# Optimization experiments

Measured on AMD Instinct MI355X. Metric: run time of the kernel, lower is better.

Reference implementation:

```python
import jax, jax.numpy as jnp
import numpy as np

BN_EPS = 1e-5


def setup_inputs() -> dict:
    key = jax.random.key(0)
    ks = jax.random.split(key, 6)
    N, E, D_IN, D_OUT = 100000, 625000, 128, 128
    x = jax.random.normal(ks[0], (N, D_IN), dtype=jnp.float32)
    edge_index = jax.random.randint(ks[1], (2, E), 0, N, dtype=jnp.int64)
    # Glorot-style init for GCNConv weight, uniform for linear (values only matter for correctness testing)
    W = jax.random.normal(ks[2], (D_IN, D_OUT), dtype=jnp.float32) * (1.0 / np.sqrt(D_IN))
    b = jnp.zeros((D_OUT,), dtype=jnp.float32)
    res_W = jax.random.normal(ks[3], (D_IN, D_OUT), dtype=jnp.float32) * (1.0 / np.sqrt(D_IN))
    res_b = jnp.zeros((D_OUT,), dtype=jnp.float32)
    bn_gamma = jnp.ones((D_OUT,), dtype=jnp.float32)
    bn_beta = jnp.zeros((D_OUT,), dtype=jnp.float32)
    return {"x": x, "edge_index": edge_index, "W": W, "b": b,
            "res_W": res_W, "res_b": res_b, "bn_gamma": bn_gamma, "bn_beta": bn_beta}


def _gcn_forward(x, edge_index, W, b, res_W, res_b, bn_gamma, bn_beta):
    N = x.shape[0]
    # ---- GCNConv: add self-loops, symmetric degree normalization (PyG defaults) ----
    loops = jnp.arange(N, dtype=edge_index.dtype)
    src = jnp.concatenate([edge_index[0], loops])  # row (source)
    dst = jnp.concatenate([edge_index[1], loops])  # col (target)
    ones = jnp.ones(src.shape[0], dtype=x.dtype)
    deg = jax.ops.segment_sum(ones, dst, num_segments=N)  # in-degree incl. self-loop
    deg_inv_sqrt = jnp.where(deg > 0, jax.lax.rsqrt(deg), 0.0)
    norm = deg_inv_sqrt[src] * deg_inv_sqrt[dst]  # [E+N]
    # transform first (dense GEMM), then gather/scale/scatter-add
    h = x @ W  # [N, D_OUT]
    msg = h[src] * norm[:, None]  # gather + scale
    agg = jax.ops.segment_sum(msg, dst, num_segments=N) + b  # scatter-add + bias
    # ---- residual: relu(linear(x)) ----
    res = jax.nn.relu(x @ res_W + res_b)
    y = agg + res
    # ---- dropout(p=0.0) is identity; BatchNorm1d (training mode, batch stats) ----
    mean = jnp.mean(y, axis=0)
    var = jnp.mean(jnp.square(y - mean), axis=0)  # biased variance, as in torch BN normalization
    y = (y - mean) * jax.lax.rsqrt(var + BN_EPS) * bn_gamma + bn_beta
    return y


def reference(x, edge_index, W, b, res_W, res_b, bn_gamma, bn_beta):
    return _gcn_forward(x, edge_index, W, b, res_W, res_b, bn_gamma, bn_beta)
```

## Files before the change

kernel.cpp:

```cpp
#include <hip/hip_runtime.h>
#include <math.h>

#define D 128

typedef __attribute__((ext_vector_type(8))) short bf16x8;
typedef __attribute__((ext_vector_type(4))) float f32x4;
union U4 { uint4 u; bf16x8 f; };

__device__ __forceinline__ float blo(unsigned p){ return __uint_as_float(p << 16); }
__device__ __forceinline__ float bhi(unsigned p){ return __uint_as_float(p & 0xffff0000u); }
__device__ __forceinline__ unsigned bpack(float a, float b){
  unsigned x = __float_as_uint(a), y = __float_as_uint(b);
  x += 0x7fffu + ((x >> 16) & 1u);
  y += 0x7fffu + ((y >> 16) & 1u);
  return (x >> 16) | (y & 0xffff0000u);
}


__global__ void k_deg(const int* __restrict__ ei, int* __restrict__ cnt, int E){
  int e = blockIdx.x*256 + threadIdx.x;
  if (e < E) atomicAdd(cnt + ei[E + e], 1);
}

__global__ void k_scan1(const int* __restrict__ cnt, int* __restrict__ off,
                        int* __restrict__ bsum, int N){
  __shared__ int sm[256];
  int i = blockIdx.x*256 + threadIdx.x;
  int v = (i < N) ? cnt[i] : 0;
  int acc = v;
  sm[threadIdx.x] = acc;
  __syncthreads();
  for (int s = 1; s < 256; s <<= 1){
    int t = (threadIdx.x >= s) ? sm[threadIdx.x - s] : 0;
    __syncthreads();
    acc += t;
    sm[threadIdx.x] = acc;
    __syncthreads();
  }
  if (i < N) off[i] = acc - v;
  if (threadIdx.x == 255) bsum[blockIdx.x] = acc;
}

__global__ void k_scan2(int* __restrict__ bsum, int nb){
  __shared__ int sm[512];
  int v = (threadIdx.x < nb) ? bsum[threadIdx.x] : 0;
  int acc = v;
  sm[threadIdx.x] = acc;
  __syncthreads();
  for (int s = 1; s < 512; s <<= 1){
    int t = (threadIdx.x >= s) ? sm[threadIdx.x - s] : 0;
    __syncthreads();
    acc += t;
    sm[threadIdx.x] = acc;
    __syncthreads();
  }
  if (threadIdx.x < nb) bsum[threadIdx.x] = acc - v;
}

__global__ void k_scan3(int* __restrict__ off, const int* __restrict__ bsum,
                        int* __restrict__ cursor, int N){
  int i = blockIdx.x*256 + threadIdx.x;
  if (i < N){
    int o = off[i] + bsum[blockIdx.x];
    off[i] = o;
    cursor[i] = o;
  }
}

__global__ void k_prep(const float* __restrict__ x, const int* __restrict__ cnt,
                       unsigned* __restrict__ out_u, int N){
  int idx = blockIdx.x*256 + threadIdx.x;
  if (idx >= N*32) return;
  int row = idx >> 5, q = idx & 31;
  float dis = rsqrtf((float)(cnt[row] + 1));
  float4 xv = reinterpret_cast<const float4*>(x)[idx];
  uint2 r; r.x = bpack(xv.x*dis, xv.y*dis); r.y = bpack(xv.z*dis, xv.w*dis);
  reinterpret_cast<uint2*>(out_u)[(size_t)row*64 + 32 + q] = r;
}

__global__ void k_wprep(const float* __restrict__ W, const float* __restrict__ RW,
                        unsigned* __restrict__ dst){
  int idx = blockIdx.x*256 + threadIdx.x;
  int m = idx >> 13;
  int w = idx & 8191;
  int c = w >> 6, kd = w & 63;
  const float* src = m ? RW : W;
  float a = src[(2*kd)*128 + c];
  float b = src[(2*kd+1)*128 + c];
  dst[(m<<13) + c*64 + (kd ^ ((c & 7) << 2))] = bpack(a, b);
}

__global__ void k_fill(const int* __restrict__ ei, int* __restrict__ cursor,
                       int* __restrict__ elist, int E){
  int e = blockIdx.x*256 + threadIdx.x;
  if (e < E){
    int d = ei[E + e];
    int pos = atomicAdd(cursor + d, 1);
    elist[pos] = ei[e];
  }
}

__global__ __launch_bounds__(256) void k_agg(unsigned* __restrict__ out_u,
    const int* __restrict__ elist, const int* __restrict__ off,
    const int* __restrict__ cnt, int N){
  const int lane = threadIdx.x & 63;
  int wid = blockIdx.x*4 + (threadIdx.x >> 6);
  const int nw = gridDim.x*4;
  for (int i = wid; i < N; i += nw){
    int node = __builtin_amdgcn_readfirstlane(i);
    int o = off[node];
    int c = cnt[node];
    unsigned ps = out_u[(size_t)node*128 + 64 + lane];
    float a0 = 0.f, a1 = 0.f;
    for (int j0 = 0; j0 < c; j0 += 64){
      int m = c - j0; if (m > 64) m = 64;
      int li = lane < m ? lane : m-1;
      int sid = elist[o + j0 + li];
      for (int jj = 0; jj < m; jj += 4){
        int s0 = __shfl(sid, jj);
        int s1 = __shfl(sid, jj+1 < m ? jj+1 : m-1);
        int s2 = __shfl(sid, jj+2 < m ? jj+2 : m-1);
        int s3 = __shfl(sid, jj+3 < m ? jj+3 : m-1);
        unsigned p0 = out_u[(size_t)s0*128 + 64 + lane];
        unsigned p1 = out_u[(size_t)s1*128 + 64 + lane];
        unsigned p2 = out_u[(size_t)s2*128 + 64 + lane];
        unsigned p3 = out_u[(size_t)s3*128 + 64 + lane];
        if (jj+1 >= m) p1 = 0;
        if (jj+2 >= m) p2 = 0;
        if (jj+3 >= m) p3 = 0;
        a0 += blo(p0) + blo(p1) + blo(p2) + blo(p3);
        a1 += bhi(p0) + bhi(p1) + bhi(p2) + bhi(p3);
      }
    }
    a0 += blo(ps); a1 += bhi(ps);
    float dis = rsqrtf((float)(c + 1));
    out_u[(size_t)node*128 + lane] = bpack(a0*dis, a1*dis);
  }
}

__global__ __launch_bounds__(512) void k_gemm(
    const unsigned* __restrict__ wsW,
    const float* __restrict__ bias, const float* __restrict__ rbias,
    const int* __restrict__ cnt,
    float* __restrict__ out, float* __restrict__ colsum, int N)
{
  __shared__ unsigned lds[16384];
  unsigned* out_u = reinterpret_cast<unsigned*>(out);
  for (int i = threadIdx.x; i < 16384; i += 512) lds[i] = wsW[i];
  __syncthreads();

  const int lane = threadIdx.x & 63;
  const int wave = threadIdx.x >> 6;
  const int lo = lane & 15, hi = lane >> 4;
  const int rowbase = blockIdx.x * 128 + wave * 16;

  int arow = rowbase + lo; if (arow >= N) arow = N - 1;
  U4 aggF[4], xbF[4];
  #pragma unroll
  for (int kk = 0; kk < 4; ++kk){
    aggF[kk].u = *(const uint4*)&out_u[(size_t)arow*128 + kk*16 + hi*4];
    xbF[kk].u  = *(const uint4*)&out_u[(size_t)arow*128 + 64 + kk*16 + hi*4];
  }

  f32x4 accA[8], accR[8];
  #pragma unroll
  for (int ct = 0; ct < 8; ++ct){
    accA[ct] = (f32x4){0.f,0.f,0.f,0.f};
    accR[ct] = (f32x4){0.f,0.f,0.f,0.f};
  }
  #pragma unroll
  for (int ct = 0; ct < 8; ++ct){
    const int c = ct*16 + lo;
    #pragma unroll
    for (int kk = 0; kk < 4; ++kk){
      int kd = (kk*16 + hi*4) ^ ((c & 7) << 2);
      U4 wf, rf;
      wf.u = *(const uint4*)&lds[c*64 + kd];
      rf.u = *(const uint4*)&lds[8192 + c*64 + kd];
      accA[ct] = __builtin_amdgcn_mfma_f32_16x16x32_bf16(aggF[kk].f, wf.f, accA[ct], 0,0,0);
      accR[ct] = __builtin_amdgcn_mfma_f32_16x16x32_bf16(xbF[kk].f, rf.f, accR[ct], 0,0,0);
    }
  }

  float s_[4];
  #pragma unroll
  for (int j = 0; j < 4; ++j){
    int r = rowbase + hi*4 + j;
    int rc = r < N ? r : N - 1;
    s_[j] = sqrtf((float)(cnt[rc] + 1));
  }
  const int rb4 = rowbase + hi*4;
  float cs[8], cq[8];
  #pragma unroll
  for (int ct = 0; ct < 8; ++ct){
    cs[ct] = 0.f; cq[ct] = 0.f;
    float bc  = bias[ct*16 + lo];
    float rbc = rbias[ct*16 + lo];
    #pragma unroll
    for (int j = 0; j < 4; ++j){
      float y = accA[ct][j] + bc + fmaxf(accR[ct][j]*s_[j] + rbc, 0.f);
      if (rb4 + j < N){ cs[ct] += y; cq[ct] += y*y; }
      accA[ct][j] = y;
    }
  }

  __syncthreads();
  float* yl = reinterpret_cast<float*>(lds);
  #pragma unroll
  for (int ct = 0; ct < 8; ++ct){
    #pragma unroll
    for (int j = 0; j < 4; ++j)
      yl[(wave*16 + hi*4 + j)*128 + ct*16 + lo] = accA[ct][j];
  }
  __syncthreads();

  const int rbB = blockIdx.x * 128;
  #pragma unroll
  for (int chunk = 0; chunk < 16; ++chunk){
    int g = chunk*512 + threadIdx.x;
    int lr = g >> 6, d = g & 63;
    int row = rbB + lr;
    if (row < N){
      float a = yl[lr*128 + 2*d], b = yl[lr*128 + 2*d + 1];
      out_u[(size_t)row*128 + d] = bpack(a, b);
    }
  }

  #pragma unroll
  for (int ct = 0; ct < 8; ++ct){
    cs[ct] += __shfl_xor(cs[ct], 16); cs[ct] += __shfl_xor(cs[ct], 32);
    cq[ct] += __shfl_xor(cq[ct], 16); cq[ct] += __shfl_xor(cq[ct], 32);
  }
  __syncthreads();
  float* red = reinterpret_cast<float*>(lds);
  if (lane < 16){
    #pragma unroll
    for (int ct = 0; ct < 8; ++ct){
      int col = ct*16 + lane;
      red[wave*256 + 2*col]     = cs[ct];
      red[wave*256 + 2*col + 1] = cq[ct];
    }
  }
  __syncthreads();
  if (threadIdx.x < 256){
    float t = 0.f;
    #pragma unroll
    for (int w = 0; w < 8; ++w) t += red[w*256 + threadIdx.x];
    atomicAdd(colsum + threadIdx.x, t);
  }
}

__global__ __launch_bounds__(256) void k_norm(float* out, const float* __restrict__ colsum,
                       const float* __restrict__ gamma, const float* __restrict__ beta,
                       float fN, int N){
  __shared__ float sc[256];
  if (threadIdx.x < 128){
    int c = threadIdx.x;
    float mean = colsum[2*c] / fN;
    float var  = fmaxf(colsum[2*c + 1] / fN - mean*mean, 0.f);
    float s = gamma[c] * rsqrtf(var + 1e-5f);
    sc[c] = s;
    sc[128 + c] = beta[c] - mean * s;
  }
  __syncthreads();
  const int lane = threadIdx.x & 63;
  const int wv   = threadIdx.x >> 6;
  unsigned* out_u = reinterpret_cast<unsigned*>(out);
  const int rowsPerIter = gridDim.x * 16;
  for (int r0 = (blockIdx.x*4 + wv)*4; r0 < N; r0 += rowsPerIter){
    int rr = r0 + (lane >> 4);
    int d  = (lane & 15) * 4;
    if (rr < N){
      uint4 p = *reinterpret_cast<uint4*>(&out_u[(size_t)rr*128 + d]);
      int c0 = d*2;
      float4 o1, o2;
      o1.x = blo(p.x)*sc[c0+0] + sc[128+c0+0];
      o1.y = bhi(p.x)*sc[c0+1] + sc[128+c0+1];
      o1.z = blo(p.y)*sc[c0+2] + sc[128+c0+2];
      o1.w = bhi(p.y)*sc[c0+3] + sc[128+c0+3];
      o2.x = blo(p.z)*sc[c0+4] + sc[128+c0+4];
      o2.y = bhi(p.z)*sc[c0+5] + sc[128+c0+5];
      o2.z = blo(p.w)*sc[c0+6] + sc[128+c0+6];
      o2.w = bhi(p.w)*sc[c0+7] + sc[128+c0+7];
      *reinterpret_cast<float4*>(&out[(size_t)rr*128 + c0])     = o1;
      *reinterpret_cast<float4*>(&out[(size_t)rr*128 + c0 + 4]) = o2;
    }
  }
}

extern "C" void kernel_launch(void* const* d_in, const int* in_sizes, int n_in,
                              void* d_out, int out_size, void* d_ws, size_t ws_size,
                              hipStream_t stream){
  const float* x     = (const float*)d_in[0];
  const int*   ei    = (const int*)d_in[1];
  const float* W     = (const float*)d_in[2];
  const float* b     = (const float*)d_in[3];
  const float* RW    = (const float*)d_in[4];
  const float* rb    = (const float*)d_in[5];
  const float* gamma = (const float*)d_in[6];
  const float* beta  = (const float*)d_in[7];
  float* out = (float*)d_out;
  unsigned* out_u = (unsigned*)d_out;
  const int N = in_sizes[0] / D;
  const int E = in_sizes[1] / 2;

  char* ws = (char*)d_ws;
  size_t o = 0;
  auto alloc = [&](size_t bytes)->void*{
    void* p = ws + o;
    o += (bytes + 255) & ~size_t(255);
    return p;
  };
  int*      cnt    = (int*)alloc((size_t)N*4);
  int*      off    = (int*)alloc((size_t)N*4);
  int*      cursor = (int*)alloc((size_t)N*4);
  int*      bsum   = (int*)alloc(512*4);
  float*    colsum = (float*)alloc(256*4);
  unsigned* wsW    = (unsigned*)alloc(16384*4);
  int*      elist  = (int*)alloc((size_t)E*4);

  hipMemsetAsync(cnt, 0, (size_t)N*4, stream);
  hipMemsetAsync(colsum, 0, 256*4, stream);

  int egrid = (E + 255)/256;
  int nb = (N + 255)/256;
  k_deg  <<<egrid, 256, 0, stream>>>(ei, cnt, E);
  k_scan1<<<nb,    256, 0, stream>>>(cnt, off, bsum, N);
  k_scan2<<<1,     512, 0, stream>>>(bsum, nb);
  k_scan3<<<nb,    256, 0, stream>>>(off, bsum, cursor, N);
  k_prep <<<(N*32 + 255)/256, 256, 0, stream>>>(x, cnt, out_u, N);
  k_wprep<<<64,    256, 0, stream>>>(W, RW, wsW);
  k_fill <<<egrid, 256, 0, stream>>>(ei, cursor, elist, E);
  k_agg  <<<4096,  256, 0, stream>>>(out_u, elist, off, cnt, N);
  k_gemm <<<(N + 127)/128, 512, 0, stream>>>(wsW, b, rb, cnt, out, colsum, N);
  k_norm <<<2048,  256, 0, stream>>>(out, colsum, gamma, beta, (float)N, N);
}
```

Before: 271.6 us.

## Fuse prep kernels, shard CSR fill by destination, and widen aggregation loads

```diff
diff --git a/kernel.cpp b/kernel.cpp
--- a/kernel.cpp
+++ b/kernel.cpp
@@ -22,8 +22,21 @@
   if (e < E) atomicAdd(cnt + ei[E + e], 1);
 }
 
-__global__ void k_scan1(const int* __restrict__ cnt, int* __restrict__ off,
-                        int* __restrict__ bsum, int N){
+__global__ void k_scan1w(const int* __restrict__ cnt, int* __restrict__ off,
+                         int* __restrict__ bsum, int N, int nb,
+                         const float* __restrict__ W, const float* __restrict__ RW,
+                         unsigned* __restrict__ wdst){
+  if (blockIdx.x >= nb){
+    int idx = (blockIdx.x - nb)*256 + threadIdx.x;
+    int m = idx >> 13;
+    int w = idx & 8191;
+    int c = w >> 6, kd = w & 63;
+    const float* src = m ? RW : W;
+    float a = src[(2*kd)*128 + c];
+    float b = src[(2*kd+1)*128 + c];
+    wdst[(m<<13) + c*64 + (kd ^ ((c & 7) << 2))] = bpack(a, b);
+    return;
+  }
   __shared__ int sm[256];
   int i = blockIdx.x*256 + threadIdx.x;
   int v = (i < N) ? cnt[i] : 0;
@@ -57,46 +70,36 @@
   if (threadIdx.x < nb) bsum[threadIdx.x] = acc - v;
 }
 
-__global__ void k_scan3(int* __restrict__ off, const int* __restrict__ bsum,
-                        int* __restrict__ cursor, int N){
-  int i = blockIdx.x*256 + threadIdx.x;
-  if (i < N){
-    int o = off[i] + bsum[blockIdx.x];
-    off[i] = o;
-    cursor[i] = o;
-  }
-}
-
-__global__ void k_prep(const float* __restrict__ x, const int* __restrict__ cnt,
-                       unsigned* __restrict__ out_u, int N){
+__global__ void k_prep3(const float* __restrict__ x, const int* __restrict__ cnt,
+                        const int* __restrict__ bsum, int* __restrict__ off,
+                        int* __restrict__ cursor, unsigned* __restrict__ out_u, int N){
   int idx = blockIdx.x*256 + threadIdx.x;
   if (idx >= N*32) return;
   int row = idx >> 5, q = idx & 31;
+  if (q == 0){
+    int o = off[row] + bsum[row >> 8];
+    off[row] = o;
+    cursor[row] = o;
+  }
   float dis = rsqrtf((float)(cnt[row] + 1));
   float4 xv = reinterpret_cast<const float4*>(x)[idx];
   uint2 r; r.x = bpack(xv.x*dis, xv.y*dis); r.y = bpack(xv.z*dis, xv.w*dis);
   reinterpret_cast<uint2*>(out_u)[(size_t)row*64 + 32 + q] = r;
 }
 
-__global__ void k_wprep(const float* __restrict__ W, const float* __restrict__ RW,
-                        unsigned* __restrict__ dst){
-  int idx = blockIdx.x*256 + threadIdx.x;
-  int m = idx >> 13;
-  int w = idx & 8191;
-  int c = w >> 6, kd = w & 63;
-  const float* src = m ? RW : W;
-  float a = src[(2*kd)*128 + c];
-  float b = src[(2*kd+1)*128 + c];
-  dst[(m<<13) + c*64 + (kd ^ ((c & 7) << 2))] = bpack(a, b);
-}
-
-__global__ void k_fill(const int* __restrict__ ei, int* __restrict__ cursor,
-                       int* __restrict__ elist, int E){
-  int e = blockIdx.x*256 + threadIdx.x;
-  if (e < E){
+__global__ __launch_bounds__(256) void k_fill(const int* __restrict__ ei,
+    int* __restrict__ cursor, int* __restrict__ elist, int E, int N){
+  const int shard = blockIdx.x & 7;
+  const int lo = (int)(((long long)N * shard) >> 3);
+  const int hi = (int)(((long long)N * (shard + 1)) >> 3);
+  const int nbs = gridDim.x >> 3;
+  const int bi  = blockIdx.x >> 3;
+  for (int e = bi*256 + threadIdx.x; e < E; e += nbs*256){
     int d = ei[E + e];
-    int pos = atomicAdd(cursor + d, 1);
-    elist[pos] = ei[e];
+    if (d >= lo && d < hi){
+      int pos = atomicAdd(cursor + d, 1);
+      elist[pos] = ei[e];
+    }
   }
 }
 
@@ -104,37 +107,51 @@
     const int* __restrict__ elist, const int* __restrict__ off,
     const int* __restrict__ cnt, int N){
   const int lane = threadIdx.x & 63;
+  const int half = lane >> 5;
+  const int hl   = lane & 31;
   int wid = blockIdx.x*4 + (threadIdx.x >> 6);
   const int nw = gridDim.x*4;
   for (int i = wid; i < N; i += nw){
     int node = __builtin_amdgcn_readfirstlane(i);
     int o = off[node];
     int c = cnt[node];
-    unsigned ps = out_u[(size_t)node*128 + 64 + lane];
-    float a0 = 0.f, a1 = 0.f;
+    uint2 ps = *(const uint2*)&out_u[(size_t)node*128 + 64 + 2*hl];
+    float ax0=0.f, ax1=0.f, ay0=0.f, ay1=0.f;
     for (int j0 = 0; j0 < c; j0 += 64){
       int m = c - j0; if (m > 64) m = 64;
       int li = lane < m ? lane : m-1;
       int sid = elist[o + j0 + li];
-      for (int jj = 0; jj < m; jj += 4){
-        int s0 = __shfl(sid, jj);
-        int s1 = __shfl(sid, jj+1 < m ? jj+1 : m-1);
-        int s2 = __shfl(sid, jj+2 < m ? jj+2 : m-1);
-        int s3 = __shfl(sid, jj+3 < m ? jj+3 : m-1);
-        unsigned p0 = out_u[(size_t)s0*128 + 64 + lane];
-        unsigned p1 = out_u[(size_t)s1*128 + 64 + lane];
-        unsigned p2 = out_u[(size_t)s2*128 + 64 + lane];
-        unsigned p3 = out_u[(size_t)s3*128 + 64 + lane];
-        if (jj+1 >= m) p1 = 0;
-        if (jj+2 >= m) p2 = 0;
-        if (jj+3 >= m) p3 = 0;
-        a0 += blo(p0) + blo(p1) + blo(p2) + blo(p3);
-        a1 += bhi(p0) + bhi(p1) + bhi(p2) + bhi(p3);
+      for (int jj = 0; jj < m; jj += 8){
+        int n0 = jj + half, n1 = jj + 2 + half, n2 = jj + 4 + half, n3 = jj + 6 + half;
+        int s0 = __shfl(sid, n0 < m ? n0 : m-1);
+        int s1 = __shfl(sid, n1 < m ? n1 : m-1);
+        int s2 = __shfl(sid, n2 < m ? n2 : m-1);
+        int s3 = __shfl(sid, n3 < m ? n3 : m-1);
+        uint2 p0 = *(const uint2*)&out_u[(size_t)s0*128 + 64 + 2*hl];
+        uint2 p1 = *(const uint2*)&out_u[(size_t)s1*128 + 64 + 2*hl];
+        uint2 p2 = *(const uint2*)&out_u[(size_t)s2*128 + 64 + 2*hl];
+        uint2 p3 = *(const uint2*)&out_u[(size_t)s3*128 + 64 + 2*hl];
+        if (n0 >= m){ p0.x = 0; p0.y = 0; }
+        if (n1 >= m){ p1.x = 0; p1.y = 0; }
+        if (n2 >= m){ p2.x = 0; p2.y = 0; }
+        if (n3 >= m){ p3.x = 0; p3.y = 0; }
+        ax0 += blo(p0.x)+blo(p1.x)+blo(p2.x)+blo(p3.x);
+        ax1 += bhi(p0.x)+bhi(p1.x)+bhi(p2.x)+bhi(p3.x);
+        ay0 += blo(p0.y)+blo(p1.y)+blo(p2.y)+blo(p3.y);
+        ay1 += bhi(p0.y)+bhi(p1.y)+bhi(p2.y)+bhi(p3.y);
       }
     }
-    a0 += blo(ps); a1 += bhi(ps);
+    if (half == 0){
+      ax0 += blo(ps.x); ax1 += bhi(ps.x);
+      ay0 += blo(ps.y); ay1 += bhi(ps.y);
+    }
+    ax0 += __shfl_xor(ax0, 32); ax1 += __shfl_xor(ax1, 32);
+    ay0 += __shfl_xor(ay0, 32); ay1 += __shfl_xor(ay1, 32);
     float dis = rsqrtf((float)(c + 1));
-    out_u[(size_t)node*128 + lane] = bpack(a0*dis, a1*dis);
+    if (half == 0){
+      uint2 r; r.x = bpack(ax0*dis, ax1*dis); r.y = bpack(ay0*dis, ay1*dis);
+      *(uint2*)&out_u[(size_t)node*128 + 2*hl] = r;
+    }
   }
 }
 
@@ -311,27 +328,24 @@
     o += (bytes + 255) & ~size_t(255);
     return p;
   };
+  float*    colsum = (float*)alloc(256*4);
   int*      cnt    = (int*)alloc((size_t)N*4);
   int*      off    = (int*)alloc((size_t)N*4);
   int*      cursor = (int*)alloc((size_t)N*4);
   int*      bsum   = (int*)alloc(512*4);
-  float*    colsum = (float*)alloc(256*4);
   unsigned* wsW    = (unsigned*)alloc(16384*4);
   int*      elist  = (int*)alloc((size_t)E*4);
 
-  hipMemsetAsync(cnt, 0, (size_t)N*4, stream);
-  hipMemsetAsync(colsum, 0, 256*4, stream);
+  hipMemsetAsync(ws, 0, 1024 + (size_t)N*4, stream);
 
   int egrid = (E + 255)/256;
   int nb = (N + 255)/256;
-  k_deg  <<<egrid, 256, 0, stream>>>(ei, cnt, E);
-  k_scan1<<<nb,    256, 0, stream>>>(cnt, off, bsum, N);
-  k_scan2<<<1,     512, 0, stream>>>(bsum, nb);
-  k_scan3<<<nb,    256, 0, stream>>>(off, bsum, cursor, N);
-  k_prep <<<(N*32 + 255)/256, 256, 0, stream>>>(x, cnt, out_u, N);
-  k_wprep<<<64,    256, 0, stream>>>(W, RW, wsW);
-  k_fill <<<egrid, 256, 0, stream>>>(ei, cursor, elist, E);
-  k_agg  <<<4096,  256, 0, stream>>>(out_u, elist, off, cnt, N);
-  k_gemm <<<(N + 127)/128, 512, 0, stream>>>(wsW, b, rb, cnt, out, colsum, N);
-  k_norm <<<2048,  256, 0, stream>>>(out, colsum, gamma, beta, (float)N, N);
-}
+  k_deg   <<<egrid,   256, 0, stream>>>(ei, cnt, E);
+  k_scan1w<<<nb + 64, 256, 0, stream>>>(cnt, off, bsum, N, nb, W, RW, wsW);
+  k_scan2 <<<1,       512, 0, stream>>>(bsum, nb);
+  k_prep3 <<<(N*32 + 255)/256, 256, 0, stream>>>(x, cnt, bsum, off, cursor, out_u, N);
+  k_fill  <<<512,     256, 0, stream>>>(ei, cursor, elist, E, N);
+  k_agg   <<<4096,    256, 0, stream>>>(out_u, elist, off, cnt, N);
+  k_gemm  <<<(N + 127)/128, 512, 0, stream>>>(wsW, b, rb, cnt, out, colsum, N);
+  k_norm  <<<2048,    256, 0, stream>>>(out, colsum, gamma, beta, (float)N, N);
+}
```

Result: faster. 264.6 us (-2.6%).
